# Optimization experiments

Hardware: AMD Instinct MI355X
Metric: run time of the kernel (lower is better)

The kernel has to match this reference:

```python
import jax, jax.numpy as jnp
import numpy as np

B, T, D, E, I = 8, 8192, 128, 8, 16
EPS = 1e-5


def setup_inputs() -> dict:
    key = jax.random.key(0)
    ks = jax.random.split(key, 6)
    return {
        "x": jax.random.normal(ks[0], (B, T, D), dtype=jnp.float32),
        "ln_g": jnp.ones((D,), dtype=jnp.float32),
        "ln_b": jnp.zeros((D,), dtype=jnp.float32),
        "gate_w": jax.random.normal(ks[1], (D, E), dtype=jnp.float32) * (1.0 / np.sqrt(D)),
        "gate_b": jnp.zeros((E,), dtype=jnp.float32),
        "w1": jax.random.normal(ks[2], (E, D, I), dtype=jnp.float32),
        "w2": jax.random.normal(ks[3], (E, I, D), dtype=jnp.float32),
    }


def reference(x, ln_g, ln_b, gate_w, gate_b, w1, w2):
    # LayerNorm (torch default eps=1e-5)
    mu = jnp.mean(x, axis=-1, keepdims=True)
    var = jnp.mean(jnp.square(x - mu), axis=-1, keepdims=True)
    x_norm = (x - mu) * jax.lax.rsqrt(var + EPS) * ln_g + ln_b

    # Dense gating + softmax routing
    gating_logits = x_norm @ gate_w + gate_b          # [B,T,E]
    routing_weights = jax.nn.softmax(gating_logits, axis=-1)

    # All-expert FFN: small batched GEMMs (torch F.gelu default = exact erf)
    y = jax.nn.gelu(jnp.einsum('btc,eci->btei', x_norm, w1), approximate=False)
    moe_experts_out = jnp.einsum('btei,eic->btec', y, w2)  # [B,T,E,D]
    moe_agg = jnp.einsum('btec,bte->btc', moe_experts_out, routing_weights)

    return (x + moe_agg, gating_logits, moe_experts_out)
```

## Files before the change

kernel.cpp:

```cpp
#include <hip/hip_runtime.h>
#include <math.h>

#define O1_OFF 8388608
#define O2_OFF 8912896

typedef __attribute__((ext_vector_type(8))) short short8;
typedef __attribute__((ext_vector_type(4))) float f32x4;

static __device__ __forceinline__ unsigned short f2bf(float f) {
    unsigned u = __builtin_bit_cast(unsigned, f);
    u = (u + 0x7fffu + ((u >> 16) & 1u)) >> 16;
    return (unsigned short)u;
}

static __device__ __forceinline__ int swz(int row, int chunk) {
    return row * 256 + ((chunk ^ (row & 7)) << 4);
}

static __device__ __forceinline__ int tswz(int row, int col) {
    int chunk = (col >> 3) ^ ((row >> 1) & 6);
    return row * 256 + (chunk << 4) + ((col & 7) << 1);
}

static __device__ __forceinline__ void bar_lds() {
    asm volatile("s_waitcnt lgkmcnt(0)" ::: "memory");
    __builtin_amdgcn_s_barrier();
    asm volatile("" ::: "memory");
}

static __device__ __forceinline__ void fence_lds() {
    asm volatile("s_waitcnt lgkmcnt(0)" ::: "memory");
}

__global__ __launch_bounds__(256, 2) void moe_fused(
    const float* __restrict__ x, const float* __restrict__ ln_g,
    const float* __restrict__ ln_b, const float* __restrict__ gate_w,
    const float* __restrict__ gate_b, const float* __restrict__ w1,
    const float* __restrict__ w2, float* __restrict__ out)
{
    __shared__ __align__(16) char smem[67584];
    char* pXY = smem;
    char* pW  = smem + 16384;
    char* pTR = smem + 49152;
    float* pRW = (float*)(smem + 65536);

    const int t = threadIdx.x;
    const int l = t & 63;
    const int w = t >> 6;
    const int tok0 = blockIdx.x * 64;

    const int colq = (t & 31) * 4;
    const int rsub = t >> 5;

    const int rb = w * 16;
    const int col = l & 15;
    const int ak = l >> 4;
    const int arow = rb + col;

    float4 xv[8];
    {
        const float* xb = x + (size_t)tok0 * 128;
        #pragma unroll
        for (int s = 0; s < 8; ++s)
            xv[s] = *(const float4*)(xb + s * 1024 + t * 4);
    }
    float4 g4 = *(const float4*)(ln_g + colq);
    float4 b4 = *(const float4*)(ln_b + colq);

    const int e2 = t >> 5;
    unsigned pk[4][8];
    {
        #pragma unroll
        for (int cc = 0; cc < 4; ++cc)
            #pragma unroll
            for (int q = 0; q < 8; ++q) pk[cc][q] = 0u;
        const float* w2b = w2 + e2 * 2048 + colq;
        #pragma unroll
        for (int i = 0; i < 16; ++i) {
            float4 q4 = *(const float4*)(w2b + i * 128);
            unsigned sh = (i & 1) * 16;
            pk[0][i >> 1] |= (unsigned)f2bf(q4.x) << sh;
            pk[1][i >> 1] |= (unsigned)f2bf(q4.y) << sh;
            pk[2][i >> 1] |= (unsigned)f2bf(q4.z) << sh;
            pk[3][i >> 1] |= (unsigned)f2bf(q4.w) << sh;
        }
    }

    {
        const int p = t & 127, ch = t >> 7;
        const float* w1b = w1 + (p >> 4) * 2048 + (p & 15);
        #pragma unroll
        for (int cc = 0; cc < 8; ++cc) {
            short8 v;
            #pragma unroll
            for (int j = 0; j < 8; ++j)
                v[j] = (short)f2bf(w1b[(ch * 64 + cc * 8 + j) * 16]);
            *(short8*)(pW + swz(p, ch * 8 + cc)) = v;
        }
    }

    short8 gfr[4];
    float4 gb4;
    {
        #pragma unroll
        for (int ks = 0; ks < 4; ++ks)
            #pragma unroll
            for (int j = 0; j < 8; ++j) {
                float v = (col < 8) ? gate_w[(32 * ks + 8 * ak + j) * 8 + col] : 0.0f;
                gfr[ks][j] = (short)f2bf(v);
            }
        gb4 = *(const float4*)(gate_b + (ak & 1) * 4);
    }

    #pragma unroll
    for (int s = 0; s < 8; ++s) {
        float4 v = xv[s];
        float sm = v.x + v.y + v.z + v.w;
        float sq = v.x*v.x + v.y*v.y + v.z*v.z + v.w*v.w;
        #pragma unroll
        for (int m = 1; m < 32; m <<= 1) {
            sm += __shfl_xor(sm, m, 64);
            sq += __shfl_xor(sq, m, 64);
        }
        float mu = sm * (1.0f / 128.0f);
        float var = sq * (1.0f / 128.0f) - mu * mu;
        float rs = rsqrtf(var + 1e-5f);
        float n0 = (v.x - mu) * rs * g4.x + b4.x;
        float n1 = (v.y - mu) * rs * g4.y + b4.y;
        float n2 = (v.z - mu) * rs * g4.z + b4.z;
        float n3 = (v.w - mu) * rs * g4.w + b4.w;
        unsigned lo = (unsigned)f2bf(n0) | ((unsigned)f2bf(n1) << 16);
        unsigned hi = (unsigned)f2bf(n2) | ((unsigned)f2bf(n3) << 16);
        unsigned long long dvv = (unsigned long long)lo | ((unsigned long long)hi << 32);
        int row = s * 8 + rsub;
        *(unsigned long long*)(pXY + swz(row, colq >> 3) + (colq & 7) * 2) = dvv;
    }

    bar_lds();

    const f32x4 zero4 = {0.f, 0.f, 0.f, 0.f};
    const short8 zfrag = {0, 0, 0, 0, 0, 0, 0, 0};

    short8 afr[4];
    #pragma unroll
    for (int ks = 0; ks < 4; ++ks)
        afr[ks] = *(const short8*)(pXY + swz(arow, ks * 4 + ak));

    f32x4 accg = zero4;
    #pragma unroll
    for (int ks = 0; ks < 4; ++ks)
        accg = __builtin_amdgcn_mfma_f32_16x16x32_bf16(gfr[ks], afr[ks], accg, 0, 0, 0);

    const size_t trow = (size_t)(tok0 + arow);
    {
        float lg0 = accg[0] + gb4.x;
        float lg1 = accg[1] + gb4.y;
        float lg2 = accg[2] + gb4.z;
        float lg3 = accg[3] + gb4.w;
        if (ak < 2) {
            f32x4 lgv = {lg0, lg1, lg2, lg3};
            *(f32x4*)(out + O1_OFF + trow * 8 + ak * 4) = lgv;
        }
        float mx = fmaxf(fmaxf(lg0, lg1), fmaxf(lg2, lg3));
        mx = fmaxf(mx, __shfl_xor(mx, 16, 64));
        float ex0 = __expf(lg0 - mx), ex1 = __expf(lg1 - mx);
        float ex2 = __expf(lg2 - mx), ex3 = __expf(lg3 - mx);
        float sm = ex0 + ex1 + ex2 + ex3;
        sm += __shfl_xor(sm, 16, 64);
        float inv = 1.0f / sm;
        if (ak < 2) {
            f32x4 pv = {ex0 * inv, ex1 * inv, ex2 * inv, ex3 * inv};
            *(f32x4*)(pRW + arow * 8 + ak * 4) = pv;
        }
    }

    f32x4 accb[8];
    #pragma unroll
    for (int nt = 0; nt < 8; ++nt) accb[nt] = zero4;
    #pragma unroll
    for (int ks = 0; ks < 4; ++ks)
        #pragma unroll
        for (int nt = 0; nt < 8; ++nt) {
            short8 wfr = *(const short8*)(pW + swz(nt * 16 + col, ks * 4 + ak));
            accb[nt] = __builtin_amdgcn_mfma_f32_16x16x32_bf16(wfr, afr[ks], accb[nt], 0, 0, 0);
        }

    #pragma unroll
    for (int nt = 0; nt < 8; ++nt) {
        float y0 = accb[nt][0], y1 = accb[nt][1], y2 = accb[nt][2], y3 = accb[nt][3];
        y0 = 0.5f * y0 * (1.0f + erff(y0 * 0.70710678118654752f));
        y1 = 0.5f * y1 * (1.0f + erff(y1 * 0.70710678118654752f));
        y2 = 0.5f * y2 * (1.0f + erff(y2 * 0.70710678118654752f));
        y3 = 0.5f * y3 * (1.0f + erff(y3 * 0.70710678118654752f));
        unsigned lo = (unsigned)f2bf(y0) | ((unsigned)f2bf(y1) << 16);
        unsigned hi = (unsigned)f2bf(y2) | ((unsigned)f2bf(y3) << 16);
        unsigned long long dv = (unsigned long long)lo | ((unsigned long long)hi << 32);
        *(unsigned long long*)(pXY + swz(arow, nt * 2 + (ak >> 1)) + (ak & 1) * 8) = dv;
    }

    bar_lds();

    #pragma unroll
    for (int cc = 0; cc < 4; ++cc) {
        int c = colq + cc;
        int rc = e2 * 128 + c;
        int a = (c >> 2) & 3;
        *(uint4*)(pW + (((rc * 2 + 0) ^ a) << 4)) =
            make_uint4(pk[cc][0], pk[cc][1], pk[cc][2], pk[cc][3]);
        *(uint4*)(pW + (((rc * 2 + 1) ^ a) << 4)) =
            make_uint4(pk[cc][4], pk[cc][5], pk[cc][6], pk[cc][7]);
    }

    bar_lds();

    f32x4 agg[8];
    #pragma unroll
    for (int nt = 0; nt < 8; ++nt) agg[nt] = zero4;

    #pragma unroll
    for (int e = 0; e < 8; ++e) {
        float rwe[4];
        #pragma unroll
        for (int r = 0; r < 4; ++r)
            rwe[r] = pRW[(rb + ak * 4 + r) * 8 + e];
        short8 alo = *(const short8*)(pXY + swz(arow, 2 * e + (ak & 1)));
        short8 af = (ak < 2) ? alo : zfrag;
        f32x4 ot[8];
        #pragma unroll
        for (int nt = 0; nt < 8; ++nt) {
            int c = nt * 16 + col;
            int rc = e * 128 + c;
            int a = (c >> 2) & 3;
            short8 blo = *(const short8*)(pW + (((rc * 2 + (ak & 1)) ^ a) << 4));
            short8 bf = (ak < 2) ? blo : zfrag;
            ot[nt] = __builtin_amdgcn_mfma_f32_16x16x32_bf16(af, bf, zero4, 0, 0, 0);
            #pragma unroll
            for (int r = 0; r < 4; ++r)
                agg[nt][r] += rwe[r] * ot[nt][r];
        }
        #pragma unroll
        for (int nt = 0; nt < 8; ++nt)
            #pragma unroll
            for (int r = 0; r < 4; ++r)
                *(unsigned short*)(pTR + tswz(rb + ak * 4 + r, nt * 16 + col)) = f2bf(ot[nt][r]);
        fence_lds();
        #pragma unroll
        for (int i2 = 0; i2 < 8; ++i2) {
            int row = rb + i2 * 2 + (l >> 5);
            int c0 = (l & 31) * 4;
            unsigned long long raw = *(const unsigned long long*)(pTR + tswz(row, c0));
            unsigned lo = (unsigned)raw, hi = (unsigned)(raw >> 32);
            f32x4 v;
            v[0] = __builtin_bit_cast(float, lo << 16);
            v[1] = __builtin_bit_cast(float, lo & 0xffff0000u);
            v[2] = __builtin_bit_cast(float, hi << 16);
            v[3] = __builtin_bit_cast(float, hi & 0xffff0000u);
            __builtin_nontemporal_store(v,
                (f32x4*)(out + O2_OFF + (size_t)(tok0 + row) * 1024 + e * 128 + c0));
        }
        asm volatile("" ::: "memory");
    }

    bar_lds();

    #pragma unroll
    for (int nt = 0; nt < 8; ++nt) {
        int c = nt * 16 + col;
        #pragma unroll
        for (int r = 0; r < 4; ++r) {
            int row = rb + ak * 4 + r;
            *(float*)(pW + row * 512 + ((c << 2) ^ ((row & 4) << 2))) = agg[nt][r];
        }
    }

    bar_lds();

    #pragma unroll
    for (int s = 0; s < 8; ++s) {
        int row = s * 8 + rsub;
        f32x4 a4 = *(const f32x4*)(pW + row * 512 + ((colq << 2) ^ ((row & 4) << 2)));
        f32x4 o;
        o[0] = xv[s].x + a4[0];
        o[1] = xv[s].y + a4[1];
        o[2] = xv[s].z + a4[2];
        o[3] = xv[s].w + a4[3];
        __builtin_nontemporal_store(o,
            (f32x4*)(out + (size_t)(tok0 + row) * 128 + colq));
    }
}

extern "C" void kernel_launch(void* const* d_in, const int* in_sizes, int n_in,
                              void* d_out, int out_size, void* d_ws, size_t ws_size,
                              hipStream_t stream) {
    const float* x      = (const float*)d_in[0];
    const float* ln_g   = (const float*)d_in[1];
    const float* ln_b   = (const float*)d_in[2];
    const float* gate_w = (const float*)d_in[3];
    const float* gate_b = (const float*)d_in[4];
    const float* w1     = (const float*)d_in[5];
    const float* w2     = (const float*)d_in[6];
    float* out = (float*)d_out;
    (void)in_sizes; (void)n_in; (void)out_size; (void)d_ws; (void)ws_size;
    moe_fused<<<dim3(1024), dim3(256), 0, stream>>>(x, ln_g, ln_b, gate_w, gate_b, w1, w2, out);
}
```

Measured before the change: 78.86 us.

## Precompute bf16 swizzled weight images in a prep kernel, copy into LDS

Adds a small prep kernel that converts w1, w2 and gate_w to bf16 once per call and writes them in the swizzled LDS layout to workspace. Each block of the main kernel then does straight 16-byte copies from workspace into LDS instead of strided fp32 gathers and per-element conversions. This removes redundant conversion work and uncoalesced loads that all 1024 blocks repeated. In exchange it adds a second kernel launch and a serial dependency between the two kernels.

After: 80.33 us, median of 2. Within noise of the previous version (+1.9%).

```diff
diff --git a/kernel.cpp b/kernel.cpp
--- a/kernel.cpp
+++ b/kernel.cpp
@@ -3,6 +3,9 @@
 
 #define O1_OFF 8388608
 #define O2_OFF 8912896
+
+#define WS_W2T 32768
+#define WS_GFR 65536
 
 typedef __attribute__((ext_vector_type(8))) short short8;
 typedef __attribute__((ext_vector_type(4))) float f32x4;
@@ -32,11 +35,61 @@
     asm volatile("s_waitcnt lgkmcnt(0)" ::: "memory");
 }
 
+__global__ __launch_bounds__(256) void moe_prep(
+    const float* __restrict__ gate_w, const float* __restrict__ w1,
+    const float* __restrict__ w2, char* __restrict__ ws)
+{
+    const int t = threadIdx.x;
+    const int b = blockIdx.x;
+    if (b < 4) {
+        const int p = t & 127, ch = t >> 7;
+        const float* w1b = w1 + (p >> 4) * 2048 + (p & 15);
+        #pragma unroll
+        for (int q = 0; q < 2; ++q) {
+            int cc = 2 * b + q;
+            short8 v;
+            #pragma unroll
+            for (int j = 0; j < 8; ++j)
+                v[j] = (short)f2bf(w1b[(ch * 64 + cc * 8 + j) * 16]);
+            *(short8*)(ws + swz(p, ch * 8 + cc)) = v;
+        }
+        if (b == 0 && t < 64) {
+            const int col = t & 15, ak = t >> 4;
+            #pragma unroll
+            for (int ks = 0; ks < 4; ++ks) {
+                short8 v;
+                #pragma unroll
+                for (int j = 0; j < 8; ++j) {
+                    float f = (col < 8) ? gate_w[(32 * ks + 8 * ak + j) * 8 + col] : 0.0f;
+                    v[j] = (short)f2bf(f);
+                }
+                *(short8*)(ws + WS_GFR + t * 64 + ks * 16) = v;
+            }
+        }
+    } else {
+        const int e2 = t >> 5, colq = (t & 31) * 4;
+        const int cc = b - 4;
+        const int c = colq + cc;
+        const float* w2b = w2 + e2 * 2048 + c;
+        unsigned pkc[8];
+        #pragma unroll
+        for (int q = 0; q < 8; ++q) pkc[q] = 0u;
+        #pragma unroll
+        for (int i = 0; i < 16; ++i)
+            pkc[i >> 1] |= (unsigned)f2bf(w2b[i * 128]) << ((i & 1) * 16);
+        const int rc = e2 * 128 + c;
+        const int a = (c >> 2) & 3;
+        *(uint4*)(ws + WS_W2T + (((rc * 2 + 0) ^ a) << 4)) =
+            make_uint4(pkc[0], pkc[1], pkc[2], pkc[3]);
+        *(uint4*)(ws + WS_W2T + (((rc * 2 + 1) ^ a) << 4)) =
+            make_uint4(pkc[4], pkc[5], pkc[6], pkc[7]);
+    }
+}
+
 __global__ __launch_bounds__(256, 2) void moe_fused(
     const float* __restrict__ x, const float* __restrict__ ln_g,
-    const float* __restrict__ ln_b, const float* __restrict__ gate_w,
-    const float* __restrict__ gate_b, const float* __restrict__ w1,
-    const float* __restrict__ w2, float* __restrict__ out)
+    const float* __restrict__ ln_b, const float* __restrict__ gate_b,
+    const char* __restrict__ wsw, float* __restrict__ out)
 {
     __shared__ __align__(16) char smem[67584];
     char* pXY = smem;
@@ -67,50 +120,15 @@
     float4 g4 = *(const float4*)(ln_g + colq);
     float4 b4 = *(const float4*)(ln_b + colq);
 
-    const int e2 = t >> 5;
-    unsigned pk[4][8];
-    {
-        #pragma unroll
-        for (int cc = 0; cc < 4; ++cc)
-            #pragma unroll
-            for (int q = 0; q < 8; ++q) pk[cc][q] = 0u;
-        const float* w2b = w2 + e2 * 2048 + colq;
-        #pragma unroll
-        for (int i = 0; i < 16; ++i) {
-            float4 q4 = *(const float4*)(w2b + i * 128);
-            unsigned sh = (i & 1) * 16;
-            pk[0][i >> 1] |= (unsigned)f2bf(q4.x) << sh;
-            pk[1][i >> 1] |= (unsigned)f2bf(q4.y) << sh;
-            pk[2][i >> 1] |= (unsigned)f2bf(q4.z) << sh;
-            pk[3][i >> 1] |= (unsigned)f2bf(q4.w) << sh;
-        }
-    }
-
-    {
-        const int p = t & 127, ch = t >> 7;
-        const float* w1b = w1 + (p >> 4) * 2048 + (p & 15);
-        #pragma unroll
-        for (int cc = 0; cc < 8; ++cc) {
-            short8 v;
-            #pragma unroll
-            for (int j = 0; j < 8; ++j)
-                v[j] = (short)f2bf(w1b[(ch * 64 + cc * 8 + j) * 16]);
-            *(short8*)(pW + swz(p, ch * 8 + cc)) = v;
-        }
-    }
+    #pragma unroll
+    for (int k = 0; k < 8; ++k)
+        *(uint4*)(pW + t * 16 + k * 4096) = *(const uint4*)(wsw + t * 16 + k * 4096);
 
     short8 gfr[4];
-    float4 gb4;
-    {
-        #pragma unroll
-        for (int ks = 0; ks < 4; ++ks)
-            #pragma unroll
-            for (int j = 0; j < 8; ++j) {
-                float v = (col < 8) ? gate_w[(32 * ks + 8 * ak + j) * 8 + col] : 0.0f;
-                gfr[ks][j] = (short)f2bf(v);
-            }
-        gb4 = *(const float4*)(gate_b + (ak & 1) * 4);
-    }
+    #pragma unroll
+    for (int ks = 0; ks < 4; ++ks)
+        gfr[ks] = *(const short8*)(wsw + WS_GFR + l * 64 + ks * 16);
+    float4 gb4 = *(const float4*)(gate_b + (ak & 1) * 4);
 
     #pragma unroll
     for (int s = 0; s < 8; ++s) {
@@ -201,15 +219,8 @@
     bar_lds();
 
     #pragma unroll
-    for (int cc = 0; cc < 4; ++cc) {
-        int c = colq + cc;
-        int rc = e2 * 128 + c;
-        int a = (c >> 2) & 3;
-        *(uint4*)(pW + (((rc * 2 + 0) ^ a) << 4)) =
-            make_uint4(pk[cc][0], pk[cc][1], pk[cc][2], pk[cc][3]);
-        *(uint4*)(pW + (((rc * 2 + 1) ^ a) << 4)) =
-            make_uint4(pk[cc][4], pk[cc][5], pk[cc][6], pk[cc][7]);
-    }
+    for (int k = 0; k < 8; ++k)
+        *(uint4*)(pW + t * 16 + k * 4096) = *(const uint4*)(wsw + WS_W2T + t * 16 + k * 4096);
 
     bar_lds();
 
@@ -300,6 +311,8 @@
     const float* w1     = (const float*)d_in[5];
     const float* w2     = (const float*)d_in[6];
     float* out = (float*)d_out;
-    (void)in_sizes; (void)n_in; (void)out_size; (void)d_ws; (void)ws_size;
-    moe_fused<<<dim3(1024), dim3(256), 0, stream>>>(x, ln_g, ln_b, gate_w, gate_b, w1, w2, out);
-}
+    char* ws = (char*)d_ws;
+    (void)in_sizes; (void)n_in; (void)out_size; (void)ws_size;
+    moe_prep<<<dim3(8), dim3(256), 0, stream>>>(gate_w, w1, w2, ws);
+    moe_fused<<<dim3(1024), dim3(256), 0, stream>>>(x, ln_g, ln_b, gate_b, ws, out);
+}
```
